# Optimization experiments

Measured on AMD Instinct MI355X. Metric: run time of the kernel, lower is better.

## Reference

```python
import jax, jax.numpy as jnp
import numpy as np

N, E, F_IN, H, C, ED, NODES = 25000, 100000, 16, 4, 280, 6, 6


def setup_inputs() -> dict:
    key = jax.random.key(0)
    ks = jax.random.split(key, 16)
    s = lambda k, sh: jax.random.normal(k, sh, dtype=jnp.float32) * 0.05
    return {
        "x": jax.random.normal(ks[0], (N, F_IN), dtype=jnp.float32),
        "edge_index": jax.random.randint(ks[1], (2, E), 0, N, dtype=jnp.int64),
        "edge_attr": jax.random.normal(ks[2], (E, ED), dtype=jnp.float32),
        # TransformerConv params (PyG): lin_query/key/value (bias), lin_edge (no bias), lin_skip (bias)
        "Wq": s(ks[3], (F_IN, H * C)), "bq": jnp.zeros((H * C,), jnp.float32),
        "Wk": s(ks[4], (F_IN, H * C)), "bk": jnp.zeros((H * C,), jnp.float32),
        "Wv": s(ks[5], (F_IN, H * C)), "bv": jnp.zeros((H * C,), jnp.float32),
        "We": s(ks[6], (ED, H * C)),
        "Wskip": s(ks[7], (F_IN, C)), "bskip": jnp.zeros((C,), jnp.float32),
        # MLP: 280 -> 64 -> 16 -> NODES, softmax
        "W1": s(ks[8], (280, 64)), "b1": jnp.zeros((64,), jnp.float32),
        "W2": s(ks[9], (64, 16)), "b2": jnp.zeros((16,), jnp.float32),
        "W3": s(ks[10], (16, NODES)), "b3": jnp.zeros((NODES,), jnp.float32),
    }


def reference(x, edge_index, edge_attr, Wq, bq, Wk, bk, Wv, bv, We, Wskip, bskip, W1, b1, W2, b2, W3, b3):
    n = x.shape[0]
    src, dst = edge_index[0], edge_index[1]  # message j -> i (PyG convention)
    q = (x @ Wq + bq).reshape(n, H, C)
    k = (x @ Wk + bk).reshape(n, H, C)
    v = (x @ Wv + bv).reshape(n, H, C)
    e = (edge_attr @ We).reshape(-1, H, C)  # [E,H,C]
    kj = k[src] + e                          # gather + edge features
    alpha = jnp.einsum('ehc,ehc->eh', q[dst], kj) / jnp.sqrt(jnp.float32(C))  # [E,H]
    # numerically stable segment softmax over destination nodes
    amax = jax.ops.segment_max(alpha, dst, num_segments=n)
    ex = jnp.exp(alpha - amax[dst])
    denom = jax.ops.segment_sum(ex, dst, num_segments=n)
    attn = ex / (denom[dst] + 1e-16)
    out = jax.ops.segment_sum(attn[..., None] * (v[src] + e), dst, num_segments=n)  # [N,H,C]
    out = out.mean(axis=1)                  # concat=False -> mean over heads
    out = out + x @ Wskip + bskip           # root/skip connection
    h = out.reshape(-1, 280)
    h = jax.nn.relu(h @ W1 + b1)
    h = jax.nn.relu(h @ W2 + b2)
    return jax.nn.softmax(h @ W3 + b3, axis=-1)
```

## Files before the change

kernel.cpp:

```cpp
#include <hip/hip_runtime.h>

#define N_NODES 25000
#define N_EDGES 100000
#define CH 280
#define HC 1120
#define CAP 32

typedef unsigned int uint;
typedef unsigned short ushort;
typedef __attribute__((ext_vector_type(8))) short short8;
typedef __attribute__((ext_vector_type(4))) float f32x4;

#define FAC_A 0
#define FAC_B 1024
#define FAC_C 1408
#define FAC_D 1472
#define FAC_F 1536
#define FAC_G 1560
#define FAC_TOTAL 1564

#define WC_K 128

#define P_FAC_END  25
#define P_WC_END   57
#define P_W2_END   58
#define P_TOTAL    449

__device__ __forceinline__ ushort f2bf(float f) {
  union { float f; uint u; } c; c.f = f;
  uint u = c.u + 0x7FFFu + ((c.u >> 16) & 1u);
  return (ushort)(u >> 16);
}

__global__ __launch_bounds__(256) void prep_kernel(
    const float* __restrict__ Wq, const float* __restrict__ Wk,
    const float* __restrict__ We, const float* __restrict__ bq,
    const float* __restrict__ bk, float* __restrict__ fac,
    const float* __restrict__ Wv, const float* __restrict__ bv,
    const float* __restrict__ Wskip, const float* __restrict__ bskip,
    const float* __restrict__ W1, const float* __restrict__ b1,
    ushort* __restrict__ Wct,
    const float* __restrict__ W2, ushort* __restrict__ W2tg,
    const int* __restrict__ ei, const float* __restrict__ ea,
    int* __restrict__ cursor, const int* __restrict__ probe,
    float* __restrict__ erec) {
  int b = blockIdx.x;
  int tid = threadIdx.x;
  if (b < P_FAC_END) {
    int t4 = b * 256 + tid;
    int q = t4 >> 2, li = t4 & 3;
    if (q >= FAC_TOTAL) return;
    const float *pa, *pb;
    if (q < FAC_B) {
      int h = q >> 8, f = (q >> 4) & 15, g = q & 15;
      pa = Wq + f * HC + h * CH; pb = Wk + g * HC + h * CH;
    } else if (q < FAC_C) {
      int u = q - FAC_B; int h = u / 96, v2 = u % 96, f = v2 / 6, j = v2 % 6;
      pa = Wq + f * HC + h * CH; pb = We + j * HC + h * CH;
    } else if (q < FAC_D) {
      int u = q - FAC_C; int h = u >> 4, f = u & 15;
      pa = Wq + f * HC + h * CH; pb = bk + h * CH;
    } else if (q < FAC_F) {
      int u = q - FAC_D; int h = u >> 4, g = u & 15;
      pa = Wk + g * HC + h * CH; pb = bq + h * CH;
    } else if (q < FAC_G) {
      int u = q - FAC_F; int h = u / 6, j = u % 6;
      pa = We + j * HC + h * CH; pb = bq + h * CH;
    } else {
      int h = q - FAC_G;
      pa = bq + h * CH; pb = bk + h * CH;
    }
    float acc = 0.f;
    int c0 = li * 70;
    for (int c = c0; c < c0 + 70; ++c) acc = fmaf(pa[c], pb[c], acc);
    acc += __shfl_xor(acc, 1);
    acc += __shfl_xor(acc, 2);
    if (li == 0) fac[q] = acc;
  } else if (b < P_WC_END) {
    int wid = tid >> 6;
    int r = __builtin_amdgcn_readfirstlane((b - P_FAC_END) * 4 + wid);
    int k = tid & 63;
    float v = 0.f;
    bool wz = true;
    if (r < 113) {
      const float* w = nullptr;
      float scale = 1.f;
      bool zero = false;
      if (r < 96) {
        int h = r / 24, j = r % 24;
        if (j == 23) zero = true;
        else {
          if (j < 16) w = Wv + j * HC + h * CH;
          else if (j < 22) w = We + (j - 16) * HC + h * CH;
          else w = bv + h * CH;
          scale = 0.25f;
        }
      } else if (r < 112) {
        w = Wskip + (r - 96) * CH;
      } else {
        w = bskip;
      }
      if (!zero) {
        float acc = 0.f;
        for (int c = 0; c < CH; ++c) acc = fmaf(w[c], W1[c * 64 + k], acc);
        v = acc * scale;
        if (r == 112) v += b1[k];
        wz = false;
      }
    }
    Wct[k * WC_K + r] = wz ? (ushort)0 : f2bf(v);
  } else if (b < P_W2_END) {
    for (int t = tid; t < 1024; t += 256) {
      int m2 = t >> 6, k = t & 63;
      W2tg[m2 * 64 + k] = f2bf(W2[(size_t)k * 16 + m2]);
    }
  } else {
    int e = (b - P_W2_END) * 256 + tid;
    if (e >= N_EDGES) return;
    int src = ei[e];
    int dst = ei[N_EDGES + e];
    int base = *probe;
    int pos = atomicAdd(&cursor[dst], 1) - base;
    if (pos >= CAP) return;
    const float2* s2 = (const float2*)(ea + (size_t)e * 6);
    float2 e01 = s2[0], e23 = s2[1], e45 = s2[2];
    int4 w0;
    w0.x = src;
    w0.y = __float_as_int(e01.x); w0.z = __float_as_int(e01.y);
    w0.w = __float_as_int(e23.x);
    float4 w1 = make_float4(e23.y, e45.x, e45.y, 0.f);
    float* dstp = erec + ((size_t)dst * CAP + pos) * 8;
    *(int4*)dstp = w0;
    *(float4*)(dstp + 4) = w1;
  }
}

__global__ __launch_bounds__(256, 2) void fused_kernel(
    const float* __restrict__ x, const float* __restrict__ fac,
    const float* __restrict__ erec, const int* __restrict__ cursor,
    const int* __restrict__ probe,
    const ushort* __restrict__ Wct, const ushort* __restrict__ W2tg,
    const float* __restrict__ b2, const float* __restrict__ W3,
    const float* __restrict__ b3, float* __restrict__ out) {
  __shared__ ushort Vls[64 * 136];
  __shared__ ushort Wcs[64 * 136];
  __shared__ ushort W2ts[16 * 72];
  __shared__ ushort h1b[64 * 72];
  __shared__ float  h2s[64 * 17];
  const float RS = 0.05976143046671968f;
  int tid = threadIdx.x;
  int wid = tid >> 6, lane = tid & 63;
  int h = __builtin_amdgcn_readfirstlane(wid);

  {
    int row = tid >> 2, seg = tid & 3;
    const ushort* src = Wct + row * 128 + seg * 32;
    ushort* dst = Wcs + row * 136 + seg * 32;
#pragma unroll
    for (int i = 0; i < 4; ++i)
      *(int4*)(dst + i * 8) = *(const int4*)(src + i * 8);
  }
  if (tid < 128) {
    int row = tid >> 3, seg = tid & 7;
    *(int4*)(W2ts + row * 72 + seg * 8) = *(const int4*)(W2tg + row * 64 + seg * 8);
  }

  int n0 = blockIdx.x * 64 + lane;
  bool valid = n0 < N_NODES;
  int n = valid ? n0 : (N_NODES - 1);
  float xv[16];
  {
    const float4* x4 = (const float4*)(x + (size_t)n * 16);
#pragma unroll
    for (int i = 0; i < 4; ++i) {
      float4 q = x4[i];
      xv[4 * i] = q.x; xv[4 * i + 1] = q.y; xv[4 * i + 2] = q.z; xv[4 * i + 3] = q.w;
    }
  }
  const float* Af = fac + FAC_A + h * 256;
  const float* Bf = fac + FAC_B + h * 96;
  const float* cf = fac + FAC_C + h * 16;
  const float* df = fac + FAC_D + h * 16;
  const float* ff = fac + FAC_F + h * 6;
  const float  gf = fac[FAC_G + h];
  float va[16];
#pragma unroll
  for (int g = 0; g < 16; ++g) {
    float a = df[g];
#pragma unroll
    for (int f = 0; f < 16; ++f) a = fmaf(xv[f], Af[f * 16 + g], a);
    va[g] = a;
  }
  float ve[6];
#pragma unroll
  for (int j = 0; j < 6; ++j) {
    float a = ff[j];
#pragma unroll
    for (int f = 0; f < 16; ++f) a = fmaf(xv[f], Bf[f * 6 + j], a);
    ve[j] = a;
  }
  float v22 = gf;
#pragma unroll
  for (int f = 0; f < 16; ++f) v22 = fmaf(xv[f], cf[f], v22);

  int base = *probe;
  int dg = valid ? (cursor[n0] - base) : 0;
  if (dg > CAP) dg = CAP;
  float m = -1e30f, den = 0.f;
  float Sx[16];
  float Sa[6];
#pragma unroll
  for (int f = 0; f < 16; ++f) Sx[f] = 0.f;
#pragma unroll
  for (int j = 0; j < 6; ++j) Sa[j] = 0.f;
  for (int q2 = 0; q2 < dg; ++q2) {
    const float* er = erec + ((size_t)n0 * CAP + q2) * 8;
    int4 ra = *(const int4*)er;
    float4 rb = *(const float4*)(er + 4);
    int s = ra.x;
    const float4* xs4 = (const float4*)(x + (size_t)s * 16);
    float4 a0 = xs4[0], a1 = xs4[1], a2 = xs4[2], a3 = xs4[3];
    float xs[16] = {a0.x, a0.y, a0.z, a0.w, a1.x, a1.y, a1.z, a1.w,
                    a2.x, a2.y, a2.z, a2.w, a3.x, a3.y, a3.z, a3.w};
    float eav[6] = {__int_as_float(ra.y), __int_as_float(ra.z),
                    __int_as_float(ra.w), rb.x, rb.y, rb.z};
    float alpha = v22;
#pragma unroll
    for (int f = 0; f < 16; ++f) alpha = fmaf(va[f], xs[f], alpha);
#pragma unroll
    for (int j = 0; j < 6; ++j) alpha = fmaf(ve[j], eav[j], alpha);
    alpha *= RS;
    float nm = fmaxf(m, alpha);
    float sc = __expf(m - nm);
    float w = __expf(alpha - nm);
    den = den * sc + w;
#pragma unroll
    for (int f = 0; f < 16; ++f) Sx[f] = fmaf(Sx[f], sc, w * xs[f]);
#pragma unroll
    for (int j = 0; j < 6; ++j) Sa[j] = fmaf(Sa[j], sc, w * eav[j]);
    m = nm;
  }
  {
    float inv = 1.f / (den + 1e-16f);
    float outv[24];
#pragma unroll
    for (int f = 0; f < 16; ++f) outv[f] = Sx[f] * inv;
#pragma unroll
    for (int j = 0; j < 6; ++j) outv[16 + j] = Sa[j] * inv;
    outv[22] = den * inv;
    outv[23] = 0.f;
    uint pk[12];
#pragma unroll
    for (int i = 0; i < 12; ++i)
      pk[i] = (uint)f2bf(outv[2 * i]) | ((uint)f2bf(outv[2 * i + 1]) << 16);
    int4* vp = (int4*)(Vls + lane * 136 + h * 24);
    int4 s0, s1, s2;
    s0.x = (int)pk[0]; s0.y = (int)pk[1]; s0.z = (int)pk[2]; s0.w = (int)pk[3];
    s1.x = (int)pk[4]; s1.y = (int)pk[5]; s1.z = (int)pk[6]; s1.w = (int)pk[7];
    s2.x = (int)pk[8]; s2.y = (int)pk[9]; s2.z = (int)pk[10]; s2.w = (int)pk[11];
    vp[0] = s0; vp[1] = s1; vp[2] = s2;
  }
  if (wid == 0) {
    uint pk[8];
#pragma unroll
    for (int i = 0; i < 8; ++i)
      pk[i] = (uint)f2bf(xv[2 * i]) | ((uint)f2bf(xv[2 * i + 1]) << 16);
    int4* vp = (int4*)(Vls + lane * 136 + 96);
    int4 s0, s1, s2, s3;
    s0.x = (int)pk[0]; s0.y = (int)pk[1]; s0.z = (int)pk[2]; s0.w = (int)pk[3];
    s1.x = (int)pk[4]; s1.y = (int)pk[5]; s1.z = (int)pk[6]; s1.w = (int)pk[7];
    s2.x = (int)0x3F80u; s2.y = 0; s2.z = 0; s2.w = 0;
    s3.x = 0; s3.y = 0; s3.z = 0; s3.w = 0;
    vp[0] = s0; vp[1] = s1; vp[2] = s2; vp[3] = s3;
  }
  __syncthreads();

  int col15 = lane & 15, quad = lane >> 4;
  f32x4 acc[4];
#pragma unroll
  for (int T = 0; T < 4; ++T) acc[T] = (f32x4){0.f, 0.f, 0.f, 0.f};
#pragma unroll
  for (int kk = 0; kk < 4; ++kk) {
    int k0 = kk * 32;
    short8 a = *(const short8*)(Vls + (wid * 16 + col15) * 136 + k0 + quad * 8);
#pragma unroll
    for (int T = 0; T < 4; ++T) {
      short8 bfr = *(const short8*)(Wcs + (T * 16 + col15) * 136 + k0 + quad * 8);
      acc[T] = __builtin_amdgcn_mfma_f32_16x16x32_bf16(a, bfr, acc[T], 0, 0, 0);
    }
  }
#pragma unroll
  for (int T = 0; T < 4; ++T) {
#pragma unroll
    for (int r = 0; r < 4; ++r) {
      int nloc = wid * 16 + quad * 4 + r;
      int c = T * 16 + col15;
      h1b[nloc * 72 + c] = f2bf(fmaxf(acc[T][r], 0.f));
    }
  }
  __syncthreads();
  float b2v = b2[col15];
  f32x4 acc2 = (f32x4){0.f, 0.f, 0.f, 0.f};
#pragma unroll
  for (int kk = 0; kk < 2; ++kk) {
    int k0 = kk * 32;
    short8 a2 = *(const short8*)(h1b + (wid * 16 + col15) * 72 + k0 + quad * 8);
    short8 bf2 = *(const short8*)(W2ts + col15 * 72 + k0 + quad * 8);
    acc2 = __builtin_amdgcn_mfma_f32_16x16x32_bf16(a2, bf2, acc2, 0, 0, 0);
  }
#pragma unroll
  for (int r = 0; r < 4; ++r) {
    int nloc = wid * 16 + quad * 4 + r;
    h2s[nloc * 17 + col15] = fmaxf(acc2[r] + b2v, 0.f);
  }
  __syncthreads();
  if (tid < 64) {
    int n2 = blockIdx.x * 64 + tid;
    if (n2 < N_NODES) {
      float hv[16];
#pragma unroll
      for (int j = 0; j < 16; ++j) hv[j] = h2s[tid * 17 + j];
      float lg[6];
      float mx = -1e30f;
#pragma unroll
      for (int o = 0; o < 6; ++o) {
        float a = b3[o];
#pragma unroll
        for (int j = 0; j < 16; ++j) a = fmaf(hv[j], W3[j * 6 + o], a);
        lg[o] = a; mx = fmaxf(mx, a);
      }
      float s = 0.f;
#pragma unroll
      for (int o = 0; o < 6; ++o) { lg[o] = __expf(lg[o] - mx); s += lg[o]; }
      float inv = 1.f / s;
      float2* o2 = (float2*)(out + (size_t)n2 * 6);
      o2[0] = make_float2(lg[0] * inv, lg[1] * inv);
      o2[1] = make_float2(lg[2] * inv, lg[3] * inv);
      o2[2] = make_float2(lg[4] * inv, lg[5] * inv);
    }
  }
}

extern "C" void kernel_launch(void* const* d_in, const int* in_sizes, int n_in,
                              void* d_out, int out_size, void* d_ws, size_t ws_size,
                              hipStream_t stream) {
  const float* x     = (const float*)d_in[0];
  const int*   ei    = (const int*)d_in[1];
  const float* ea    = (const float*)d_in[2];
  const float* Wq    = (const float*)d_in[3];
  const float* bq    = (const float*)d_in[4];
  const float* Wk    = (const float*)d_in[5];
  const float* bk    = (const float*)d_in[6];
  const float* Wv    = (const float*)d_in[7];
  const float* bv    = (const float*)d_in[8];
  const float* We    = (const float*)d_in[9];
  const float* Wskip = (const float*)d_in[10];
  const float* bskip = (const float*)d_in[11];
  const float* W1    = (const float*)d_in[12];
  const float* b1    = (const float*)d_in[13];
  const float* W2    = (const float*)d_in[14];
  const float* b2    = (const float*)d_in[15];
  const float* W3    = (const float*)d_in[16];
  const float* b3    = (const float*)d_in[17];
  float* out = (float*)d_out;
  (void)in_sizes; (void)n_in; (void)out_size; (void)ws_size;

  char* ws = (char*)d_ws;
  size_t off = 0;
  auto alloc = [&](size_t bytes) {
    void* p = ws + off;
    off = (off + bytes + 255) & ~(size_t)255;
    return p;
  };
  float*  fac    = (float*)alloc(FAC_TOTAL * 4);
  ushort* Wct    = (ushort*)alloc(64 * WC_K * 2);
  int*    cursor = (int*)alloc(N_NODES * 4);
  int*    probe  = (int*)alloc(256);
  ushort* W2tg   = (ushort*)alloc(16 * 64 * 2);
  float*  erec   = (float*)alloc((size_t)N_NODES * CAP * 32);

  prep_kernel<<<P_TOTAL, 256, 0, stream>>>(
      Wq, Wk, We, bq, bk, fac, Wv, bv, Wskip, bskip, W1, b1, Wct, W2, W2tg,
      ei, ea, cursor, probe, erec);
  fused_kernel<<<391, 256, 0, stream>>>(x, fac, erec, cursor, probe, Wct, W2tg,
                                        b2, W3, b3, out);
}
```

Measured before the change: 117.0 us.

## Split each node's edge loop across two lanes and drop LDS weight staging

```diff
diff --git a/kernel.cpp b/kernel.cpp
--- a/kernel.cpp
+++ b/kernel.cpp
@@ -135,7 +135,7 @@
   }
 }
 
-__global__ __launch_bounds__(256, 2) void fused_kernel(
+__global__ __launch_bounds__(512, 2) void fused_kernel(
     const float* __restrict__ x, const float* __restrict__ fac,
     const float* __restrict__ erec, const int* __restrict__ cursor,
     const int* __restrict__ probe,
@@ -143,29 +143,17 @@
     const float* __restrict__ b2, const float* __restrict__ W3,
     const float* __restrict__ b3, float* __restrict__ out) {
   __shared__ ushort Vls[64 * 136];
-  __shared__ ushort Wcs[64 * 136];
-  __shared__ ushort W2ts[16 * 72];
   __shared__ ushort h1b[64 * 72];
   __shared__ float  h2s[64 * 17];
   const float RS = 0.05976143046671968f;
   int tid = threadIdx.x;
   int wid = tid >> 6, lane = tid & 63;
-  int h = __builtin_amdgcn_readfirstlane(wid);
-
-  {
-    int row = tid >> 2, seg = tid & 3;
-    const ushort* src = Wct + row * 128 + seg * 32;
-    ushort* dst = Wcs + row * 136 + seg * 32;
-#pragma unroll
-    for (int i = 0; i < 4; ++i)
-      *(int4*)(dst + i * 8) = *(const int4*)(src + i * 8);
-  }
-  if (tid < 128) {
-    int row = tid >> 3, seg = tid & 7;
-    *(int4*)(W2ts + row * 72 + seg * 8) = *(const int4*)(W2tg + row * 64 + seg * 8);
-  }
-
-  int n0 = blockIdx.x * 64 + lane;
+  int h = __builtin_amdgcn_readfirstlane(wid & 3);
+  int nb = __builtin_amdgcn_readfirstlane(wid >> 2);
+  int nloc = nb * 32 + (lane >> 1);
+  int half = lane & 1;
+
+  int n0 = blockIdx.x * 64 + nloc;
   bool valid = n0 < N_NODES;
   int n = valid ? n0 : (N_NODES - 1);
   float xv[16];
@@ -213,7 +201,7 @@
   for (int f = 0; f < 16; ++f) Sx[f] = 0.f;
 #pragma unroll
   for (int j = 0; j < 6; ++j) Sa[j] = 0.f;
-  for (int q2 = 0; q2 < dg; ++q2) {
+  for (int q2 = half; q2 < dg; q2 += 2) {
     const float* er = erec + ((size_t)n0 * CAP + q2) * 8;
     int4 ra = *(const int4*)er;
     float4 rb = *(const float4*)(er + 4);
@@ -241,6 +229,24 @@
     m = nm;
   }
   {
+    float mo  = __shfl_xor(m, 1);
+    float dno = __shfl_xor(den, 1);
+    float mm = fmaxf(m, mo);
+    float sa = __expf(m - mm);
+    float sb = __expf(mo - mm);
+    den = den * sa + dno * sb;
+#pragma unroll
+    for (int f = 0; f < 16; ++f) {
+      float so = __shfl_xor(Sx[f], 1);
+      Sx[f] = Sx[f] * sa + so * sb;
+    }
+#pragma unroll
+    for (int j = 0; j < 6; ++j) {
+      float so = __shfl_xor(Sa[j], 1);
+      Sa[j] = Sa[j] * sa + so * sb;
+    }
+  }
+  if (half == 0) {
     float inv = 1.f / (den + 1e-16f);
     float outv[24];
 #pragma unroll
@@ -253,65 +259,69 @@
 #pragma unroll
     for (int i = 0; i < 12; ++i)
       pk[i] = (uint)f2bf(outv[2 * i]) | ((uint)f2bf(outv[2 * i + 1]) << 16);
-    int4* vp = (int4*)(Vls + lane * 136 + h * 24);
+    int4* vp = (int4*)(Vls + nloc * 136 + h * 24);
     int4 s0, s1, s2;
     s0.x = (int)pk[0]; s0.y = (int)pk[1]; s0.z = (int)pk[2]; s0.w = (int)pk[3];
     s1.x = (int)pk[4]; s1.y = (int)pk[5]; s1.z = (int)pk[6]; s1.w = (int)pk[7];
     s2.x = (int)pk[8]; s2.y = (int)pk[9]; s2.z = (int)pk[10]; s2.w = (int)pk[11];
     vp[0] = s0; vp[1] = s1; vp[2] = s2;
-  }
-  if (wid == 0) {
-    uint pk[8];
-#pragma unroll
-    for (int i = 0; i < 8; ++i)
-      pk[i] = (uint)f2bf(xv[2 * i]) | ((uint)f2bf(xv[2 * i + 1]) << 16);
-    int4* vp = (int4*)(Vls + lane * 136 + 96);
-    int4 s0, s1, s2, s3;
-    s0.x = (int)pk[0]; s0.y = (int)pk[1]; s0.z = (int)pk[2]; s0.w = (int)pk[3];
-    s1.x = (int)pk[4]; s1.y = (int)pk[5]; s1.z = (int)pk[6]; s1.w = (int)pk[7];
-    s2.x = (int)0x3F80u; s2.y = 0; s2.z = 0; s2.w = 0;
-    s3.x = 0; s3.y = 0; s3.z = 0; s3.w = 0;
-    vp[0] = s0; vp[1] = s1; vp[2] = s2; vp[3] = s3;
+    if (h == 0) {
+      uint pq[8];
+#pragma unroll
+      for (int i = 0; i < 8; ++i)
+        pq[i] = (uint)f2bf(xv[2 * i]) | ((uint)f2bf(xv[2 * i + 1]) << 16);
+      int4* vq = (int4*)(Vls + nloc * 136 + 96);
+      int4 t0, t1, t2, t3;
+      t0.x = (int)pq[0]; t0.y = (int)pq[1]; t0.z = (int)pq[2]; t0.w = (int)pq[3];
+      t1.x = (int)pq[4]; t1.y = (int)pq[5]; t1.z = (int)pq[6]; t1.w = (int)pq[7];
+      t2.x = (int)0x3F80u; t2.y = 0; t2.z = 0; t2.w = 0;
+      t3.x = 0; t3.y = 0; t3.z = 0; t3.w = 0;
+      vq[0] = t0; vq[1] = t1; vq[2] = t2; vq[3] = t3;
+    }
   }
   __syncthreads();
 
   int col15 = lane & 15, quad = lane >> 4;
-  f32x4 acc[4];
-#pragma unroll
-  for (int T = 0; T < 4; ++T) acc[T] = (f32x4){0.f, 0.f, 0.f, 0.f};
-#pragma unroll
-  for (int kk = 0; kk < 4; ++kk) {
-    int k0 = kk * 32;
-    short8 a = *(const short8*)(Vls + (wid * 16 + col15) * 136 + k0 + quad * 8);
+  if (wid < 4) {
+    f32x4 acc[4];
+#pragma unroll
+    for (int T = 0; T < 4; ++T) acc[T] = (f32x4){0.f, 0.f, 0.f, 0.f};
+#pragma unroll
+    for (int kk = 0; kk < 4; ++kk) {
+      int k0 = kk * 32;
+      short8 a = *(const short8*)(Vls + (wid * 16 + col15) * 136 + k0 + quad * 8);
+#pragma unroll
+      for (int T = 0; T < 4; ++T) {
+        short8 bfr = *(const short8*)(Wct + (T * 16 + col15) * WC_K + k0 + quad * 8);
+        acc[T] = __builtin_amdgcn_mfma_f32_16x16x32_bf16(a, bfr, acc[T], 0, 0, 0);
+      }
+    }
 #pragma unroll
     for (int T = 0; T < 4; ++T) {
-      short8 bfr = *(const short8*)(Wcs + (T * 16 + col15) * 136 + k0 + quad * 8);
-      acc[T] = __builtin_amdgcn_mfma_f32_16x16x32_bf16(a, bfr, acc[T], 0, 0, 0);
-    }
-  }
-#pragma unroll
-  for (int T = 0; T < 4; ++T) {
+#pragma unroll
+      for (int r = 0; r < 4; ++r) {
+        int nl = wid * 16 + quad * 4 + r;
+        int c = T * 16 + col15;
+        h1b[nl * 72 + c] = f2bf(fmaxf(acc[T][r], 0.f));
+      }
+    }
+  }
+  __syncthreads();
+  if (wid < 4) {
+    float b2v = b2[col15];
+    f32x4 acc2 = (f32x4){0.f, 0.f, 0.f, 0.f};
+#pragma unroll
+    for (int kk = 0; kk < 2; ++kk) {
+      int k0 = kk * 32;
+      short8 a2 = *(const short8*)(h1b + (wid * 16 + col15) * 72 + k0 + quad * 8);
+      short8 bf2 = *(const short8*)(W2tg + col15 * 64 + k0 + quad * 8);
+      acc2 = __builtin_amdgcn_mfma_f32_16x16x32_bf16(a2, bf2, acc2, 0, 0, 0);
+    }
 #pragma unroll
     for (int r = 0; r < 4; ++r) {
-      int nloc = wid * 16 + quad * 4 + r;
-      int c = T * 16 + col15;
-      h1b[nloc * 72 + c] = f2bf(fmaxf(acc[T][r], 0.f));
-    }
-  }
-  __syncthreads();
-  float b2v = b2[col15];
-  f32x4 acc2 = (f32x4){0.f, 0.f, 0.f, 0.f};
-#pragma unroll
-  for (int kk = 0; kk < 2; ++kk) {
-    int k0 = kk * 32;
-    short8 a2 = *(const short8*)(h1b + (wid * 16 + col15) * 72 + k0 + quad * 8);
-    short8 bf2 = *(const short8*)(W2ts + col15 * 72 + k0 + quad * 8);
-    acc2 = __builtin_amdgcn_mfma_f32_16x16x32_bf16(a2, bf2, acc2, 0, 0, 0);
-  }
-#pragma unroll
-  for (int r = 0; r < 4; ++r) {
-    int nloc = wid * 16 + quad * 4 + r;
-    h2s[nloc * 17 + col15] = fmaxf(acc2[r] + b2v, 0.f);
+      int nl = wid * 16 + quad * 4 + r;
+      h2s[nl * 17 + col15] = fmaxf(acc2[r] + b2v, 0.f);
+    }
   }
   __syncthreads();
   if (tid < 64) {
@@ -382,6 +392,6 @@
   prep_kernel<<<P_TOTAL, 256, 0, stream>>>(
       Wq, Wk, We, bq, bk, fac, Wv, bv, Wskip, bskip, W1, b1, Wct, W2, W2tg,
       ei, ea, cursor, probe, erec);
-  fused_kernel<<<391, 256, 0, stream>>>(x, fac, erec, cursor, probe, Wct, W2tg,
+  fused_kernel<<<391, 512, 0, stream>>>(x, fac, erec, cursor, probe, Wct, W2tg,
                                         b2, W3, b3, out);
 }
```

Result: no change. 116.6 us (-0.3%).
